# Performance work log

Measured on AMD Instinct MI355X. Metric: run time of the kernel, lower is better.

The kernel has to match this reference:

```python
import jax, jax.numpy as jnp
import numpy as np

C, H, W = 64, 32, 32  # feature planes are (1, 64, 32, 32)
M = 1_048_576         # number of query points


def bilinear_sample(plane, coords):
    """torch.nn.functional.grid_sample, mode='bilinear', padding_mode='zeros',
    align_corners=True, for a single plane.
    plane: (C, H, W); coords: (M, 2) with (x, y) in [-1, 1] convention.
    Returns (M, C)."""
    c, h, w = plane.shape
    # align_corners=True mapping: -1 -> 0, +1 -> size-1
    x = (coords[:, 0] + 1.0) * 0.5 * (w - 1)
    y = (coords[:, 1] + 1.0) * 0.5 * (h - 1)
    x0 = jnp.floor(x)
    y0 = jnp.floor(y)
    wx1 = x - x0
    wy1 = y - y0
    wx0 = 1.0 - wx1
    wy0 = 1.0 - wy1

    def gather(xi, yi):
        xi = xi.astype(jnp.int32)
        yi = yi.astype(jnp.int32)
        valid = (xi >= 0) & (xi < w) & (yi >= 0) & (yi < h)  # zeros padding
        xc = jnp.clip(xi, 0, w - 1)
        yc = jnp.clip(yi, 0, h - 1)
        v = plane[:, yc, xc]  # (C, M)
        return jnp.where(valid[None, :], v, 0.0)

    out = (gather(x0, y0) * (wx0 * wy0)[None, :]
           + gather(x0 + 1, y0) * (wx1 * wy0)[None, :]
           + gather(x0, y0 + 1) * (wx0 * wy1)[None, :]
           + gather(x0 + 1, y0 + 1) * (wx1 * wy1)[None, :])
    return out.T  # (M, C)


def setup_inputs() -> dict:
    key = jax.random.key(0)
    ks = jax.random.split(key, 10)
    coordinates = jax.random.normal(ks[0], (1, M, 3), dtype=jnp.float32)
    # tri-plane embeddings: randn * 0.1, shape (1, C, H, W)
    plane_xy = jax.random.normal(ks[1], (1, C, H, W), dtype=jnp.float32) * 0.1
    plane_yz = jax.random.normal(ks[2], (1, C, H, W), dtype=jnp.float32) * 0.1
    plane_xz = jax.random.normal(ks[3], (1, C, H, W), dtype=jnp.float32) * 0.1
    # MLP 64 -> 128 -> 128 -> 1 (torch Linear weight shape = (out, in))
    # layer 0: first_layer_sine_init -> U(-1/64, 1/64)
    w1 = jax.random.uniform(ks[4], (128, 64), jnp.float32, -1.0 / 64, 1.0 / 64)
    b1 = jnp.zeros((128,), jnp.float32)
    # layers 1,2: frequency_init(30) -> U(-sqrt(6/in)/30, sqrt(6/in)/30)
    s2 = np.sqrt(6.0 / 128) / 30.0
    w2 = jax.random.uniform(ks[5], (128, 128), jnp.float32, -s2, s2)
    b2 = jnp.zeros((128,), jnp.float32)
    w3 = jax.random.uniform(ks[6], (1, 128), jnp.float32, -s2, s2)
    b3 = jnp.zeros((1,), jnp.float32)
    return {"coordinates": coordinates, "plane_xy": plane_xy, "plane_yz": plane_yz,
            "plane_xz": plane_xz, "w1": w1, "b1": b1, "w2": w2, "b2": b2,
            "w3": w3, "b3": b3}


def reference(coordinates, plane_xy, plane_yz, plane_xz, w1, b1, w2, b2, w3, b3):
    # coordinates: (1, M, 3); planes have leading batch dim of 1 (torch requires
    # grid batch == plane batch, so batch_size is structurally 1).
    samp = jax.vmap(bilinear_sample, in_axes=(None, 0))
    xy = samp(plane_xy[0], coordinates[..., 0:2])   # (1, M, C)
    yz = samp(plane_yz[0], coordinates[..., 1:3])   # (1, M, C)
    xz = samp(plane_xz[0], coordinates[..., ::2])   # (1, M, C)
    features = xy * yz * xz                          # aggregate_fn='prod'
    h = jax.nn.relu(jnp.einsum('bmc,oc->bmo', features, w1) + b1)
    h = jax.nn.relu(jnp.einsum('bmc,oc->bmo', h, w2) + b2)
    out = jnp.einsum('bmc,oc->bmo', h, w3) + b3      # (1, M, 1)
    return out
```

## Files before the change

### kernel.cpp

```cpp
#include <hip/hip_runtime.h>

#define MPTS 1048576

typedef _Float16 f16;
typedef _Float16 f16x2 __attribute__((ext_vector_type(2)));
typedef _Float16 f16x4 __attribute__((ext_vector_type(4)));
typedef _Float16 f16x8 __attribute__((ext_vector_type(8)));
typedef float f32x4 __attribute__((ext_vector_type(4)));

static const size_t OFF_Z    = 0;
static const size_t OFF_CNT  = 64;
static const size_t OFF_PL   = 256;
static const size_t OFF_PLD  = OFF_PL + 786432;
static const size_t OFF_W1H  = OFF_PLD + 786432;
static const size_t OFF_W2H  = OFF_W1H + 16384;
static const size_t OFF_BCNT = OFF_W2H + 32768;
static const size_t OFF_BOFF = OFF_BCNT + 4096;
static const size_t OFF_LIST = OFF_BOFF + 4096;
static const size_t OFF_PC   = OFF_LIST + (size_t)MPTS*4;
static const size_t WS_LIST  = OFF_PC;
static const size_t WS_PC    = OFF_PC + (size_t)MPTS*16;

__device__ __forceinline__ int iclamp(int v, int lo, int hi) {
    return v < lo ? lo : (v > hi ? hi : v);
}
__device__ __forceinline__ int imin(int a, int b) { return a < b ? a : b; }

__device__ __forceinline__ bool isact(float x, float y, float z) {
    float px = fmaf(x, 15.5f, 15.5f);
    float py = fmaf(y, 15.5f, 15.5f);
    float pz = fmaf(z, 15.5f, 15.5f);
    return (px > -1.0f) & (px < 32.0f) & (py > -1.0f) & (py < 32.0f) &
           (pz > -1.0f) & (pz < 32.0f);
}

struct Bi { int o00, o01, o10, o11; float w00, w01, w10, w11; };

__device__ __forceinline__ Bi mkbi(float pa, float pb) {
    float fa = floorf(pa), fb = floorf(pb);
    int ia0 = (int)fa, ib0 = (int)fb;
    int ia1 = ia0 + 1, ib1 = ib0 + 1;
    float wa1 = pa - fa, wa0 = 1.0f - wa1;
    float wb1 = pb - fb, wb0 = 1.0f - wb1;
    float va0 = (ia0 >= 0 && ia0 < 32) ? wa0 : 0.0f;
    float va1 = (ia1 >= 0 && ia1 < 32) ? wa1 : 0.0f;
    float vb0 = (ib0 >= 0 && ib0 < 32) ? wb0 : 0.0f;
    float vb1 = (ib1 >= 0 && ib1 < 32) ? wb1 : 0.0f;
    int ca0 = iclamp(ia0, 0, 31), ca1 = iclamp(ia1, 0, 31);
    int cb0 = iclamp(ib0, 0, 31), cb1 = iclamp(ib1, 0, 31);
    Bi r;
    r.o00 = (cb0 * 32 + ca0) * 64; r.o01 = (cb0 * 32 + ca1) * 64;
    r.o10 = (cb1 * 32 + ca0) * 64; r.o11 = (cb1 * 32 + ca1) * 64;
    r.w00 = va0 * vb0; r.w01 = va1 * vb0; r.w10 = va0 * vb1; r.w11 = va1 * vb1;
    return r;
}

__device__ __forceinline__ float4 lerp4d(const f16* __restrict__ base, const int4 P) {
    f16x8 r0 = *(const f16x8*)(base + P.x);
    f16x8 r1 = *(const f16x8*)(base + P.y);
    f16x2 w0 = __builtin_bit_cast(f16x2, P.z);
    f16x2 w1 = __builtin_bit_cast(f16x2, P.w);
    const f16x2* a0 = (const f16x2*)&r0;
    const f16x2* a1 = (const f16x2*)&r1;
    float4 r;
    r.x = __builtin_amdgcn_fdot2(a0[0], w0, __builtin_amdgcn_fdot2(a1[0], w1, 0.0f, false), false);
    r.y = __builtin_amdgcn_fdot2(a0[1], w0, __builtin_amdgcn_fdot2(a1[1], w1, 0.0f, false), false);
    r.z = __builtin_amdgcn_fdot2(a0[2], w0, __builtin_amdgcn_fdot2(a1[2], w1, 0.0f, false), false);
    r.w = __builtin_amdgcn_fdot2(a0[3], w0, __builtin_amdgcn_fdot2(a1[3], w1, 0.0f, false), false);
    return r;
}

__device__ __forceinline__ void samp16(const float* __restrict__ pl,
                                       float pa, float pb, int c0,
                                       float* __restrict__ f, const bool mult) {
    Bi B = mkbi(pa, pb);
    const float4* p00 = (const float4*)(pl + B.o00 + c0);
    const float4* p01 = (const float4*)(pl + B.o01 + c0);
    const float4* p10 = (const float4*)(pl + B.o10 + c0);
    const float4* p11 = (const float4*)(pl + B.o11 + c0);
#pragma unroll
    for (int q = 0; q < 4; ++q) {
        float4 g00 = p00[q], g01 = p01[q], g10 = p10[q], g11 = p11[q];
        float vx = fmaf(B.w00, g00.x, fmaf(B.w01, g01.x, fmaf(B.w10, g10.x, B.w11 * g11.x)));
        float vy = fmaf(B.w00, g00.y, fmaf(B.w01, g01.y, fmaf(B.w10, g10.y, B.w11 * g11.y)));
        float vz = fmaf(B.w00, g00.z, fmaf(B.w01, g01.z, fmaf(B.w10, g10.z, B.w11 * g11.z)));
        float vw = fmaf(B.w00, g00.w, fmaf(B.w01, g01.w, fmaf(B.w10, g10.w, B.w11 * g11.w)));
        if (mult) {
            f[4*q+0] *= vx; f[4*q+1] *= vy; f[4*q+2] *= vz; f[4*q+3] *= vw;
        } else {
            f[4*q+0] = vx; f[4*q+1] = vy; f[4*q+2] = vz; f[4*q+3] = vw;
        }
    }
}

__global__ void k_prep(const float* __restrict__ pxy, const float* __restrict__ pyz,
                       const float* __restrict__ pxz,
                       const float* __restrict__ w1, const float* __restrict__ w2,
                       const float* __restrict__ b1, const float* __restrict__ b2,
                       const float* __restrict__ w3, const float* __restrict__ b3,
                       float* __restrict__ planes, f16* __restrict__ dupl,
                       f16* __restrict__ w1h, f16* __restrict__ w2h,
                       float* __restrict__ zout) {
    if (blockIdx.x == 864) {
        int p = threadIdx.x;
        if (p >= 128) return;
        float h2p = b2[p];
        for (int o = 0; o < 128; ++o) h2p += w2[p * 128 + o] * fmaxf(b1[o], 0.0f);
        __shared__ float red[128];
        red[p] = fmaxf(h2p, 0.0f) * w3[p];
        __syncthreads();
        for (int s = 64; s > 0; s >>= 1) {
            if (p < s) red[p] += red[p + s];
            __syncthreads();
        }
        if (p == 0) *zout = red[0] + b3[0];
        return;
    }
    int tid = blockIdx.x * 256 + threadIdx.x;
    if (tid < 3 * 65536) {
        int t = tid >> 16;
        int r = tid & 65535;
        int hw = r >> 6;
        int c = r & 63;
        int y = hw >> 5, x = hw & 31;
        int xp1 = imin(x + 1, 31);
        const float* src = (t == 0) ? pxy : ((t == 1) ? pyz : pxz);
        float v  = src[c * 1024 + hw];
        float v1 = src[c * 1024 + y * 32 + xp1];
        planes[tid] = v;
        f16* d = dupl + (size_t)t * 131072 + hw * 128 + c * 2;
        d[0] = (f16)v;
        d[1] = (f16)v1;
    } else if (tid < 3 * 65536 + 8192) {
        int r = tid - 3 * 65536;
        w1h[r] = (f16)w1[r];
    } else {
        int r = tid - (3 * 65536 + 8192);
        w2h[r] = (f16)w2[r];
    }
}

__global__ void k_count(const float* __restrict__ coords, const float* __restrict__ zptr,
                        int* __restrict__ bcnt, float* __restrict__ out) {
    int t = threadIdx.x, bid = blockIdx.x;
    const float4* c4 = (const float4*)coords + 768 * (size_t)bid + 3 * t;
    float4 a = c4[0], b = c4[1], c = c4[2];
    int base = bid * 1024 + t * 4;
    float z = *zptr;
    bool a0 = isact(a.x, a.y, a.z);
    bool a1 = isact(a.w, b.x, b.y);
    bool a2 = isact(b.z, b.w, c.x);
    bool a3 = isact(c.y, c.z, c.w);
    if (!a0) out[base + 0] = z;
    if (!a1) out[base + 1] = z;
    if (!a2) out[base + 2] = z;
    if (!a3) out[base + 3] = z;
    int s = (int)a0 + (int)a1 + (int)a2 + (int)a3;
#pragma unroll
    for (int off = 1; off <= 32; off <<= 1) s += __shfl_xor(s, off, 64);
    __shared__ int wt[4];
    if ((t & 63) == 0) wt[t >> 6] = s;
    __syncthreads();
    if (t == 0) bcnt[bid] = wt[0] + wt[1] + wt[2] + wt[3];
}

__global__ void k_scan(const int* __restrict__ bcnt, int* __restrict__ boff,
                       int* __restrict__ cnt) {
    int t = threadIdx.x, lane = t & 63, wv = t >> 6;
    int mine = bcnt[t];
    int incl = mine;
#pragma unroll
    for (int off = 1; off <= 32; off <<= 1) {
        int v = __shfl_up(incl, off, 64);
        if (lane >= off) incl += v;
    }
    __shared__ int wtot[16];
    if (lane == 63) wtot[wv] = incl;
    __syncthreads();
    int wexcl = 0;
#pragma unroll
    for (int k = 0; k < 16; ++k) wexcl += (k < wv) ? wtot[k] : 0;
    boff[t] = wexcl + incl - mine;
    if (t == 1023) *cnt = wexcl + incl;
}

template<bool PC>
__global__ void k_scatter(const float* __restrict__ coords, const int* __restrict__ boff,
                          int* __restrict__ list, float4* __restrict__ pc4) {
    int t = threadIdx.x, bid = blockIdx.x, lane = t & 63, wv = t >> 6;
    const float4* c4 = (const float4*)coords + 768 * (size_t)bid + 3 * t;
    float4 a = c4[0], b = c4[1], c = c4[2];
    int base = bid * 1024 + t * 4;
    float xs[4] = {a.x, a.w, b.z, c.y};
    float ys[4] = {a.y, b.x, b.w, c.z};
    float zs[4] = {a.z, b.y, c.x, c.w};
    bool act[4];
#pragma unroll
    for (int j = 0; j < 4; ++j) act[j] = isact(xs[j], ys[j], zs[j]);
    int mine = (int)act[0] + (int)act[1] + (int)act[2] + (int)act[3];
    int incl = mine;
#pragma unroll
    for (int off = 1; off <= 32; off <<= 1) {
        int v = __shfl_up(incl, off, 64);
        if (lane >= off) incl += v;
    }
    __shared__ int wtot[4];
    if (lane == 63) wtot[wv] = incl;
    __syncthreads();
    int wexcl = 0;
#pragma unroll
    for (int k = 0; k < 4; ++k) wexcl += (k < wv) ? wtot[k] : 0;
    int pos = boff[bid] + wexcl + incl - mine;
#pragma unroll
    for (int j = 0; j < 4; ++j) {
        if (act[j]) {
            list[pos] = base + j;
            if (PC) {
                float4 p;
                p.x = fmaf(xs[j], 15.5f, 15.5f);
                p.y = fmaf(ys[j], 15.5f, 15.5f);
                p.z = fmaf(zs[j], 15.5f, 15.5f);
                p.w = 0.0f;
                pc4[pos] = p;
            }
            ++pos;
        }
    }
}

__global__ __launch_bounds__(256, 2)
void k_fused(const float4* __restrict__ pc4, const f16* __restrict__ dupl,
             const f16* __restrict__ w1h, const f16* __restrict__ w2h,
             const float* __restrict__ b1, const float* __restrict__ b2,
             const float* __restrict__ w3, const float* __restrict__ b3,
             const int* __restrict__ cnt, const int* __restrict__ list,
             float* __restrict__ out) {
    const int n = *cnt;
    const int tile = blockIdx.x;
    if (tile * 64 >= n) return;

    __shared__ __attribute__((aligned(16))) char smem[16384 + 3072];
    f16*   Fs   = (f16*)smem;
    f16*   H1s  = (f16*)smem;
    int4*  BsP  = (int4*)(smem + 16384);
    float* outp = (float*)(smem + 16384);

    const int t   = threadIdx.x;
    const int wv  = t >> 6;
    const int l   = t & 63;
    const int l15 = l & 15;
    const int lg  = l >> 4;
    const int ptw = t >> 4;
    const int cq  = t & 15;

    const float b3v = b3[0];

    if ((t & 3) < 3) {
        int pt0 = t >> 2;
        int pl  = t & 3;
        int ic = imin(tile * 64 + pt0, n - 1);
        float4 c = pc4[ic];
        float pa = (pl == 1) ? c.y : c.x;
        float pb = (pl == 0) ? c.y : c.z;
        float fa = floorf(pa), fb = floorf(pb);
        int ia0 = (int)fa, ib0 = (int)fb;
        float wa1 = pa - fa, wa0 = 1.0f - wa1;
        float wb1 = pb - fb, wb0 = 1.0f - wb1;
        float va0 = (ia0 >= 0 && ia0 < 32) ? wa0 : 0.0f;
        float va1 = (ia0 + 1 >= 0 && ia0 + 1 < 32) ? wa1 : 0.0f;
        float vb0 = (ib0 >= 0 && ib0 < 32) ? wb0 : 0.0f;
        float vb1 = (ib0 + 1 >= 0 && ib0 + 1 < 32) ? wb1 : 0.0f;
        int xb = iclamp(ia0, 0, 31);
        float wx0 = (ia0 < 0) ? va1 : va0;
        float wx1 = (ia0 < 0) ? 0.0f : va1;
        int yb0 = iclamp(ib0, 0, 31), yb1 = iclamp(ib0 + 1, 0, 31);
        f16x2 p0; p0[0] = (f16)(wx0 * vb0); p0[1] = (f16)(wx1 * vb0);
        f16x2 p1; p1[0] = (f16)(wx0 * vb1); p1[1] = (f16)(wx1 * vb1);
        int o0 = (yb0 * 32 + xb) * 128;
        int o1 = (yb1 * 32 + xb) * 128;
        BsP[pt0 * 3 + pl] = make_int4(o0, o1,
                                      __builtin_bit_cast(int, p0),
                                      __builtin_bit_cast(int, p1));
    }
    __syncthreads();

    const f16* bch = dupl + cq * 8;
#pragma unroll
    for (int pass = 0; pass < 4; ++pass) {
        int pt = pass * 16 + ptw;
        float4 s0 = lerp4d(bch,          BsP[pt * 3 + 0]);
        float4 s1 = lerp4d(bch + 131072, BsP[pt * 3 + 1]);
        float4 s2 = lerp4d(bch + 262144, BsP[pt * 3 + 2]);
        float4 f;
        f.x = (s0.x * s1.x) * s2.x;
        f.y = (s0.y * s1.y) * s2.y;
        f.z = (s0.z * s1.z) * s2.z;
        f.w = (s0.w * s1.w) * s2.w;
        f16x4 pk;
        pk[0] = (f16)f.x; pk[1] = (f16)f.y; pk[2] = (f16)f.z; pk[3] = (f16)f.w;
        *(f16x4*)((char*)Fs + pt * 128 + ((cq * 8) ^ ((pt & 7) << 4))) = pk;
    }
    __syncthreads();

    f16x8 af[4][2];
#pragma unroll
    for (int Mt = 0; Mt < 4; ++Mt) {
        int row = Mt * 16 + l15;
        const char* rb = (const char*)Fs + row * 128;
        int sw = (row & 7) << 4;
        af[Mt][0] = *(const f16x8*)(rb + ((lg * 16) ^ sw));
        af[Mt][1] = *(const f16x8*)(rb + ((64 + lg * 16) ^ sw));
    }

    f16x8 wf1[2][2];
    f16x8 wf2[2][4];
    f32x4 b1q[2], b2q[2], w3q[2];
#pragma unroll
    for (int ntl = 0; ntl < 2; ++ntl) {
        int nrow = (wv * 2 + ntl) * 16 + l15;
        wf1[ntl][0] = *(const f16x8*)(w1h + nrow * 64 + lg * 8);
        wf1[ntl][1] = *(const f16x8*)(w1h + nrow * 64 + 32 + lg * 8);
#pragma unroll
        for (int ks = 0; ks < 4; ++ks)
            wf2[ntl][ks] = *(const f16x8*)(w2h + nrow * 128 + ks * 32 + lg * 8);
        int nb = (wv * 2 + ntl) * 16 + lg * 4;
        b1q[ntl] = *(const f32x4*)(b1 + nb);
        b2q[ntl] = *(const f32x4*)(b2 + nb);
        w3q[ntl] = *(const f32x4*)(w3 + nb);
    }
    __syncthreads();

    f32x4 acc[2][4];
#pragma unroll
    for (int ntl = 0; ntl < 2; ++ntl)
#pragma unroll
        for (int Mt = 0; Mt < 4; ++Mt) acc[ntl][Mt] = b1q[ntl];
    __builtin_amdgcn_s_setprio(1);
#pragma unroll
    for (int Mt = 0; Mt < 4; ++Mt) {
#pragma unroll
        for (int ntl = 0; ntl < 2; ++ntl) {
            acc[ntl][Mt] = __builtin_amdgcn_mfma_f32_16x16x32_f16(wf1[ntl][0], af[Mt][0], acc[ntl][Mt], 0, 0, 0);
            acc[ntl][Mt] = __builtin_amdgcn_mfma_f32_16x16x32_f16(wf1[ntl][1], af[Mt][1], acc[ntl][Mt], 0, 0, 0);
        }
    }
    __builtin_amdgcn_s_setprio(0);

#pragma unroll
    for (int ntl = 0; ntl < 2; ++ntl) {
#pragma unroll
        for (int Mt = 0; Mt < 4; ++Mt) {
            int pt = Mt * 16 + l15;
            int off = (((wv * 2 + ntl) * 32 + lg * 8) ^ ((pt & 7) << 4));
            f16x4 h;
            h[0] = (f16)fmaxf(acc[ntl][Mt][0], 0.0f);
            h[1] = (f16)fmaxf(acc[ntl][Mt][1], 0.0f);
            h[2] = (f16)fmaxf(acc[ntl][Mt][2], 0.0f);
            h[3] = (f16)fmaxf(acc[ntl][Mt][3], 0.0f);
            *(f16x4*)((char*)H1s + pt * 256 + off) = h;
        }
    }
    __syncthreads();

    f32x4 acc2[2][4];
#pragma unroll
    for (int ntl = 0; ntl < 2; ++ntl)
#pragma unroll
        for (int Mt = 0; Mt < 4; ++Mt) acc2[ntl][Mt] = b2q[ntl];
#pragma unroll
    for (int Mt = 0; Mt < 4; ++Mt) {
        int row = Mt * 16 + l15;
        const char* rb = (const char*)H1s + row * 256;
        int sw = (row & 7) << 4;
        f16x8 a0 = *(const f16x8*)(rb + ((lg * 16) ^ sw));
        f16x8 a1 = *(const f16x8*)(rb + ((64 + lg * 16) ^ sw));
        f16x8 a2 = *(const f16x8*)(rb + ((128 + lg * 16) ^ sw));
        f16x8 a3 = *(const f16x8*)(rb + ((192 + lg * 16) ^ sw));
        __builtin_amdgcn_s_setprio(1);
#pragma unroll
        for (int ntl = 0; ntl < 2; ++ntl) {
            acc2[ntl][Mt] = __builtin_amdgcn_mfma_f32_16x16x32_f16(wf2[ntl][0], a0, acc2[ntl][Mt], 0, 0, 0);
            acc2[ntl][Mt] = __builtin_amdgcn_mfma_f32_16x16x32_f16(wf2[ntl][1], a1, acc2[ntl][Mt], 0, 0, 0);
            acc2[ntl][Mt] = __builtin_amdgcn_mfma_f32_16x16x32_f16(wf2[ntl][2], a2, acc2[ntl][Mt], 0, 0, 0);
            acc2[ntl][Mt] = __builtin_amdgcn_mfma_f32_16x16x32_f16(wf2[ntl][3], a3, acc2[ntl][Mt], 0, 0, 0);
        }
        __builtin_amdgcn_s_setprio(0);
    }

#pragma unroll
    for (int Mt = 0; Mt < 4; ++Mt) {
        float s = 0.0f;
#pragma unroll
        for (int ntl = 0; ntl < 2; ++ntl)
#pragma unroll
            for (int r = 0; r < 4; ++r)
                s = fmaf(fmaxf(acc2[ntl][Mt][r], 0.0f), w3q[ntl][r], s);
        s += __shfl_xor(s, 16, 64);
        s += __shfl_xor(s, 32, 64);
        if (lg == 0) outp[wv * 64 + Mt * 16 + l15] = s;
    }
    __syncthreads();
    if (t < 64) {
        int gi = tile * 64 + t;
        if (gi < n) {
            float s = outp[0 * 64 + t] + outp[1 * 64 + t] +
                      outp[2 * 64 + t] + outp[3 * 64 + t] + b3v;
            out[list[gi]] = s;
        }
    }
}

__global__ __launch_bounds__(256, 2)
void k_mlp(const float* __restrict__ coords, const float* __restrict__ planes,
           const f16* __restrict__ w1h, const f16* __restrict__ w2h,
           const float* __restrict__ b1, const float* __restrict__ b2,
           const float* __restrict__ w3, const float* __restrict__ b3,
           const int* __restrict__ cnt, const int* __restrict__ list,
           float* __restrict__ out) {
    const int n = *cnt;
    const int tile = blockIdx.x;
    if (tile * 64 >= n) return;

    __shared__ __attribute__((aligned(16))) f16 Fs[64 * 64];
    __shared__ __attribute__((aligned(16))) f16 H1s[64 * 128];
    __shared__ float outp[4][64];

    const int t   = threadIdx.x;
    const int wv  = t >> 6;
    const int l   = t & 63;
    const int l15 = l & 15;
    const int lg  = l >> 4;

    const float* pl0 = planes;
    const float* pl1 = planes + 65536;
    const float* pl2 = planes + 131072;

    f16x8 wf1[2][2];
    f16x8 wf2[2][4];
    float b1v[2], b2v[2], w3v[2];
#pragma unroll
    for (int ntl = 0; ntl < 2; ++ntl) {
        int nrow = (wv * 2 + ntl) * 16 + l15;
#pragma unroll
        for (int ks = 0; ks < 2; ++ks)
            wf1[ntl][ks] = *(const f16x8*)(w1h + nrow * 64 + ks * 32 + lg * 8);
#pragma unroll
        for (int ks = 0; ks < 4; ++ks)
            wf2[ntl][ks] = *(const f16x8*)(w2h + nrow * 128 + ks * 32 + lg * 8);
        b1v[ntl] = b1[nrow];
        b2v[ntl] = b2[nrow];
        w3v[ntl] = w3[nrow];
    }
    const float b3v = b3[0];

    {
        int pt = t >> 2, c0 = (t & 3) * 16;
        int ic = imin(tile * 64 + pt, n - 1);
        int i = list[ic];
        float px = fmaf(coords[3 * i + 0], 15.5f, 15.5f);
        float py = fmaf(coords[3 * i + 1], 15.5f, 15.5f);
        float pz = fmaf(coords[3 * i + 2], 15.5f, 15.5f);
        float feat[16];
        samp16(pl0, px, py, c0, feat, false);
        samp16(pl1, py, pz, c0, feat, true);
        samp16(pl2, px, pz, c0, feat, true);
        int sw = (pt & 7) << 4;
        char* Fb = (char*)Fs + pt * 128;
        f16x8 pk;
#pragma unroll
        for (int j = 0; j < 8; ++j) pk[j] = (f16)feat[j];
        *(f16x8*)(Fb + ((c0 * 2) ^ sw)) = pk;
#pragma unroll
        for (int j = 0; j < 8; ++j) pk[j] = (f16)feat[8 + j];
        *(f16x8*)(Fb + ((c0 * 2 + 16) ^ sw)) = pk;
    }
    __syncthreads();

    f32x4 acc[2][4];
#pragma unroll
    for (int ntl = 0; ntl < 2; ++ntl) {
        f32x4 ini = {b1v[ntl], b1v[ntl], b1v[ntl], b1v[ntl]};
#pragma unroll
        for (int Mt = 0; Mt < 4; ++Mt) acc[ntl][Mt] = ini;
    }
#pragma unroll
    for (int Mt = 0; Mt < 4; ++Mt) {
        int row = Mt * 16 + l15;
        const char* rb = (const char*)Fs + row * 128;
        int sw = (row & 7) << 4;
        f16x8 a0 = *(const f16x8*)(rb + ((lg * 16) ^ sw));
        f16x8 a1 = *(const f16x8*)(rb + ((64 + lg * 16) ^ sw));
#pragma unroll
        for (int ntl = 0; ntl < 2; ++ntl) {
            acc[ntl][Mt] = __builtin_amdgcn_mfma_f32_16x16x32_f16(a0, wf1[ntl][0], acc[ntl][Mt], 0, 0, 0);
            acc[ntl][Mt] = __builtin_amdgcn_mfma_f32_16x16x32_f16(a1, wf1[ntl][1], acc[ntl][Mt], 0, 0, 0);
        }
    }
#pragma unroll
    for (int ntl = 0; ntl < 2; ++ntl) {
        int ncol = (wv * 2 + ntl) * 16 + l15;
#pragma unroll
        for (int Mt = 0; Mt < 4; ++Mt) {
#pragma unroll
            for (int r = 0; r < 4; ++r) {
                int prow = Mt * 16 + lg * 4 + r;
                float v = fmaxf(acc[ntl][Mt][r], 0.0f);
                *(f16*)((char*)H1s + prow * 256 + ((ncol * 2) ^ ((prow & 7) << 4))) = (f16)v;
            }
        }
    }
    __syncthreads();

    f32x4 acc2[2][4];
#pragma unroll
    for (int ntl = 0; ntl < 2; ++ntl) {
        f32x4 ini = {b2v[ntl], b2v[ntl], b2v[ntl], b2v[ntl]};
#pragma unroll
        for (int Mt = 0; Mt < 4; ++Mt) acc2[ntl][Mt] = ini;
    }
#pragma unroll
    for (int Mt = 0; Mt < 4; ++Mt) {
        int row = Mt * 16 + l15;
        const char* rb = (const char*)H1s + row * 256;
        int sw = (row & 7) << 4;
        f16x8 a0 = *(const f16x8*)(rb + ((lg * 16) ^ sw));
        f16x8 a1 = *(const f16x8*)(rb + ((64 + lg * 16) ^ sw));
        f16x8 a2 = *(const f16x8*)(rb + ((128 + lg * 16) ^ sw));
        f16x8 a3 = *(const f16x8*)(rb + ((192 + lg * 16) ^ sw));
#pragma unroll
        for (int ntl = 0; ntl < 2; ++ntl) {
            acc2[ntl][Mt] = __builtin_amdgcn_mfma_f32_16x16x32_f16(a0, wf2[ntl][0], acc2[ntl][Mt], 0, 0, 0);
            acc2[ntl][Mt] = __builtin_amdgcn_mfma_f32_16x16x32_f16(a1, wf2[ntl][1], acc2[ntl][Mt], 0, 0, 0);
            acc2[ntl][Mt] = __builtin_amdgcn_mfma_f32_16x16x32_f16(a2, wf2[ntl][2], acc2[ntl][Mt], 0, 0, 0);
            acc2[ntl][Mt] = __builtin_amdgcn_mfma_f32_16x16x32_f16(a3, wf2[ntl][3], acc2[ntl][Mt], 0, 0, 0);
        }
    }

    float part[4][4];
#pragma unroll
    for (int Mt = 0; Mt < 4; ++Mt)
#pragma unroll
        for (int r = 0; r < 4; ++r)
            part[Mt][r] = fmaxf(acc2[0][Mt][r], 0.0f) * w3v[0] +
                          fmaxf(acc2[1][Mt][r], 0.0f) * w3v[1];
#pragma unroll
    for (int off = 1; off <= 8; off <<= 1) {
#pragma unroll
        for (int Mt = 0; Mt < 4; ++Mt)
#pragma unroll
            for (int r = 0; r < 4; ++r)
                part[Mt][r] += __shfl_xor(part[Mt][r], off, 64);
    }
    if (l15 == 0) {
#pragma unroll
        for (int Mt = 0; Mt < 4; ++Mt)
#pragma unroll
            for (int r = 0; r < 4; ++r)
                outp[wv][Mt * 16 + lg * 4 + r] = part[Mt][r];
    }
    __syncthreads();
    if (t < 64) {
        int gi = tile * 64 + t;
        if (gi < n) {
            float s = outp[0][t] + outp[1][t] + outp[2][t] + outp[3][t] + b3v;
            out[list[gi]] = s;
        }
    }
}

__global__ void k_fallback(const float* __restrict__ coords,
                           const float* __restrict__ p0, const float* __restrict__ p1,
                           const float* __restrict__ p2,
                           const float* __restrict__ w1, const float* __restrict__ b1,
                           const float* __restrict__ w2, const float* __restrict__ b2,
                           const float* __restrict__ w3, const float* __restrict__ b3,
                           float* __restrict__ out) {
    int i = blockIdx.x * 256 + threadIdx.x;
    if (i >= MPTS) return;
    float x = coords[3 * i + 0], y = coords[3 * i + 1], z = coords[3 * i + 2];
    float px = fmaf(x, 15.5f, 15.5f);
    float py = fmaf(y, 15.5f, 15.5f);
    float pz = fmaf(z, 15.5f, 15.5f);
    float feat[64];
    const float* pls[3] = {p0, p1, p2};
    float pa[3] = {px, py, px}, pb[3] = {py, pz, pz};
    for (int pidx = 0; pidx < 3; ++pidx) {
        float paf = pa[pidx], pbf = pb[pidx];
        float fa = floorf(paf), fb = floorf(pbf);
        int ia0 = (int)fa, ib0 = (int)fb, ia1 = ia0 + 1, ib1 = ib0 + 1;
        float wa1 = paf - fa, wa0 = 1.0f - wa1, wb1 = pbf - fb, wb0 = 1.0f - wb1;
        float va0 = (ia0 >= 0 && ia0 < 32) ? wa0 : 0.0f;
        float va1 = (ia1 >= 0 && ia1 < 32) ? wa1 : 0.0f;
        float vb0 = (ib0 >= 0 && ib0 < 32) ? wb0 : 0.0f;
        float vb1 = (ib1 >= 0 && ib1 < 32) ? wb1 : 0.0f;
        int ca0 = iclamp(ia0, 0, 31), ca1 = iclamp(ia1, 0, 31);
        int cb0 = iclamp(ib0, 0, 31), cb1 = iclamp(ib1, 0, 31);
        float w00 = va0 * vb0, w01 = va1 * vb0, w10 = va0 * vb1, w11 = va1 * vb1;
        int o00 = cb0 * 32 + ca0, o01 = cb0 * 32 + ca1;
        int o10 = cb1 * 32 + ca0, o11 = cb1 * 32 + ca1;
        const float* pl = pls[pidx];
        for (int c = 0; c < 64; ++c) {
            const float* pc = pl + c * 1024;
            float v = fmaf(w00, pc[o00], fmaf(w01, pc[o01],
                      fmaf(w10, pc[o10], w11 * pc[o11])));
            if (pidx == 0) feat[c] = v; else feat[c] *= v;
        }
    }
    float oa = b3[0];
    for (int half = 0; half < 2; ++half) {
        float h2h[64];
        for (int p = 0; p < 64; ++p) h2h[p] = b2[half * 64 + p];
        for (int o = 0; o < 128; ++o) {
            float a = b1[o];
            for (int c = 0; c < 64; ++c) a = fmaf(feat[c], w1[o * 64 + c], a);
            float r = fmaxf(a, 0.0f);
            for (int p = 0; p < 64; ++p) h2h[p] = fmaf(r, w2[(half * 64 + p) * 128 + o], h2h[p]);
        }
        for (int p = 0; p < 64; ++p) oa = fmaf(fmaxf(h2h[p], 0.0f), w3[half * 64 + p], oa);
    }
    out[i] = oa;
}

extern "C" void kernel_launch(void* const* d_in, const int* in_sizes, int n_in,
                              void* d_out, int out_size, void* d_ws, size_t ws_size,
                              hipStream_t stream) {
    const float* coords = (const float*)d_in[0];
    const float* pxy    = (const float*)d_in[1];
    const float* pyz    = (const float*)d_in[2];
    const float* pxz    = (const float*)d_in[3];
    const float* w1     = (const float*)d_in[4];
    const float* b1     = (const float*)d_in[5];
    const float* w2     = (const float*)d_in[6];
    const float* b2     = (const float*)d_in[7];
    const float* w3     = (const float*)d_in[8];
    const float* b3     = (const float*)d_in[9];
    float* out = (float*)d_out;

    if (ws_size >= WS_LIST) {
        float*  zout   = (float*)((char*)d_ws + OFF_Z);
        int*    cnt    = (int*)((char*)d_ws + OFF_CNT);
        float*  planes = (float*)((char*)d_ws + OFF_PL);
        f16*    dupl   = (f16*)((char*)d_ws + OFF_PLD);
        f16*    w1h    = (f16*)((char*)d_ws + OFF_W1H);
        f16*    w2h    = (f16*)((char*)d_ws + OFF_W2H);
        int*    bcnt   = (int*)((char*)d_ws + OFF_BCNT);
        int*    boff   = (int*)((char*)d_ws + OFF_BOFF);
        int*    list   = (int*)((char*)d_ws + OFF_LIST);
        float4* pc4    = (float4*)((char*)d_ws + OFF_PC);

        k_prep<<<865, 256, 0, stream>>>(pxy, pyz, pxz, w1, w2, b1, b2, w3, b3,
                                        planes, dupl, w1h, w2h, zout);
        k_count<<<1024, 256, 0, stream>>>(coords, zout, bcnt, out);
        k_scan<<<1, 1024, 0, stream>>>(bcnt, boff, cnt);

        if (ws_size >= WS_PC) {
            k_scatter<true><<<1024, 256, 0, stream>>>(coords, boff, list, pc4);
            k_fused<<<16384, 256, 0, stream>>>(pc4, dupl, w1h, w2h,
                                               b1, b2, w3, b3, cnt, list, out);
        } else {
            k_scatter<false><<<1024, 256, 0, stream>>>(coords, boff, list, nullptr);
            k_mlp<<<16384, 256, 0, stream>>>(coords, planes, w1h, w2h,
                                             b1, b2, w3, b3, cnt, list, out);
        }
    } else {
        k_fallback<<<4096, 256, 0, stream>>>(coords, pxy, pyz, pxz,
                                             w1, b1, w2, b2, w3, b3, out);
    }
}
```

Baseline: 84.50 us.

## Fuse count, scan and scatter into one decoupled-lookback classify kernel

Replaces the three-kernel count/scan/scatter compaction with a single pass. Each block publishes its active count to a flag array, then spins on the flags of all earlier blocks to get its output offset. This removes two launches and a second read of the coordinates, at the cost of a memset and a spin-wait that relies on earlier blocks being scheduled first (forward progress is not guaranteed). It also skips writing the fp32 plane copy when the precomputed-coordinate path is used.

```diff
diff --git a/kernel.cpp b/kernel.cpp
--- a/kernel.cpp
+++ b/kernel.cpp
@@ -14,9 +14,8 @@
 static const size_t OFF_PLD  = OFF_PL + 786432;
 static const size_t OFF_W1H  = OFF_PLD + 786432;
 static const size_t OFF_W2H  = OFF_W1H + 16384;
-static const size_t OFF_BCNT = OFF_W2H + 32768;
-static const size_t OFF_BOFF = OFF_BCNT + 4096;
-static const size_t OFF_LIST = OFF_BOFF + 4096;
+static const size_t OFF_BFLG = OFF_W2H + 32768;
+static const size_t OFF_LIST = OFF_BFLG + 4096;
 static const size_t OFF_PC   = OFF_LIST + (size_t)MPTS*4;
 static const size_t WS_LIST  = OFF_PC;
 static const size_t WS_PC    = OFF_PC + (size_t)MPTS*16;
@@ -100,7 +99,7 @@
                        const float* __restrict__ w3, const float* __restrict__ b3,
                        float* __restrict__ planes, f16* __restrict__ dupl,
                        f16* __restrict__ w1h, f16* __restrict__ w2h,
-                       float* __restrict__ zout) {
+                       float* __restrict__ zout, int wplanes) {
     if (blockIdx.x == 864) {
         int p = threadIdx.x;
         if (p >= 128) return;
@@ -127,7 +126,7 @@
         const float* src = (t == 0) ? pxy : ((t == 1) ? pyz : pxz);
         float v  = src[c * 1024 + hw];
         float v1 = src[c * 1024 + y * 32 + xp1];
-        planes[tid] = v;
+        if (wplanes) planes[tid] = v;
         f16* d = dupl + (size_t)t * 131072 + hw * 128 + c * 2;
         d[0] = (f16)v;
         d[1] = (f16)v1;
@@ -140,53 +139,12 @@
     }
 }
 
-__global__ void k_count(const float* __restrict__ coords, const float* __restrict__ zptr,
-                        int* __restrict__ bcnt, float* __restrict__ out) {
-    int t = threadIdx.x, bid = blockIdx.x;
-    const float4* c4 = (const float4*)coords + 768 * (size_t)bid + 3 * t;
-    float4 a = c4[0], b = c4[1], c = c4[2];
-    int base = bid * 1024 + t * 4;
-    float z = *zptr;
-    bool a0 = isact(a.x, a.y, a.z);
-    bool a1 = isact(a.w, b.x, b.y);
-    bool a2 = isact(b.z, b.w, c.x);
-    bool a3 = isact(c.y, c.z, c.w);
-    if (!a0) out[base + 0] = z;
-    if (!a1) out[base + 1] = z;
-    if (!a2) out[base + 2] = z;
-    if (!a3) out[base + 3] = z;
-    int s = (int)a0 + (int)a1 + (int)a2 + (int)a3;
-#pragma unroll
-    for (int off = 1; off <= 32; off <<= 1) s += __shfl_xor(s, off, 64);
-    __shared__ int wt[4];
-    if ((t & 63) == 0) wt[t >> 6] = s;
-    __syncthreads();
-    if (t == 0) bcnt[bid] = wt[0] + wt[1] + wt[2] + wt[3];
-}
-
-__global__ void k_scan(const int* __restrict__ bcnt, int* __restrict__ boff,
-                       int* __restrict__ cnt) {
-    int t = threadIdx.x, lane = t & 63, wv = t >> 6;
-    int mine = bcnt[t];
-    int incl = mine;
-#pragma unroll
-    for (int off = 1; off <= 32; off <<= 1) {
-        int v = __shfl_up(incl, off, 64);
-        if (lane >= off) incl += v;
-    }
-    __shared__ int wtot[16];
-    if (lane == 63) wtot[wv] = incl;
-    __syncthreads();
-    int wexcl = 0;
-#pragma unroll
-    for (int k = 0; k < 16; ++k) wexcl += (k < wv) ? wtot[k] : 0;
-    boff[t] = wexcl + incl - mine;
-    if (t == 1023) *cnt = wexcl + incl;
-}
-
 template<bool PC>
-__global__ void k_scatter(const float* __restrict__ coords, const int* __restrict__ boff,
-                          int* __restrict__ list, float4* __restrict__ pc4) {
+__global__ void k_classify(const float* __restrict__ coords,
+                           const float* __restrict__ zptr,
+                           int* __restrict__ bflag, int* __restrict__ cnt,
+                           int* __restrict__ list, float4* __restrict__ pc4,
+                           float* __restrict__ out) {
     int t = threadIdx.x, bid = blockIdx.x, lane = t & 63, wv = t >> 6;
     const float4* c4 = (const float4*)coords + 768 * (size_t)bid + 3 * t;
     float4 a = c4[0], b = c4[1], c = c4[2];
@@ -198,6 +156,7 @@
 #pragma unroll
     for (int j = 0; j < 4; ++j) act[j] = isact(xs[j], ys[j], zs[j]);
     int mine = (int)act[0] + (int)act[1] + (int)act[2] + (int)act[3];
+
     int incl = mine;
 #pragma unroll
     for (int off = 1; off <= 32; off <<= 1) {
@@ -205,12 +164,36 @@
         if (lane >= off) incl += v;
     }
     __shared__ int wtot[4];
+    __shared__ int pw[4];
     if (lane == 63) wtot[wv] = incl;
     __syncthreads();
+    int btot = wtot[0] + wtot[1] + wtot[2] + wtot[3];
+
+    if (t == 0) atomicExch(&bflag[bid], btot + 1);
+
+    int pre = 0;
+    for (int i = t; i < bid; i += 256) {
+        int v;
+        do { v = atomicAdd(&bflag[i], 0); } while (v == 0);
+        pre += v - 1;
+    }
+#pragma unroll
+    for (int off = 1; off <= 32; off <<= 1) pre += __shfl_xor(pre, off, 64);
+    if (lane == 0) pw[wv] = pre;
+    __syncthreads();
+    int boffv = pw[0] + pw[1] + pw[2] + pw[3];
+
+    if (bid == 1023 && t == 0) *cnt = boffv + btot;
+
+    float z = *zptr;
+#pragma unroll
+    for (int j = 0; j < 4; ++j)
+        if (!act[j]) out[base + j] = z;
+
     int wexcl = 0;
 #pragma unroll
     for (int k = 0; k < 4; ++k) wexcl += (k < wv) ? wtot[k] : 0;
-    int pos = boff[bid] + wexcl + incl - mine;
+    int pos = boffv + wexcl + incl - mine;
 #pragma unroll
     for (int j = 0; j < 4; ++j) {
         if (act[j]) {
@@ -643,22 +626,22 @@
         f16*    dupl   = (f16*)((char*)d_ws + OFF_PLD);
         f16*    w1h    = (f16*)((char*)d_ws + OFF_W1H);
         f16*    w2h    = (f16*)((char*)d_ws + OFF_W2H);
-        int*    bcnt   = (int*)((char*)d_ws + OFF_BCNT);
-        int*    boff   = (int*)((char*)d_ws + OFF_BOFF);
+        int*    bflag  = (int*)((char*)d_ws + OFF_BFLG);
         int*    list   = (int*)((char*)d_ws + OFF_LIST);
         float4* pc4    = (float4*)((char*)d_ws + OFF_PC);
-
+        const bool pc  = (ws_size >= WS_PC);
+
+        hipMemsetAsync(bflag, 0, 4096, stream);
         k_prep<<<865, 256, 0, stream>>>(pxy, pyz, pxz, w1, w2, b1, b2, w3, b3,
-                                        planes, dupl, w1h, w2h, zout);
-        k_count<<<1024, 256, 0, stream>>>(coords, zout, bcnt, out);
-        k_scan<<<1, 1024, 0, stream>>>(bcnt, boff, cnt);
-
-        if (ws_size >= WS_PC) {
-            k_scatter<true><<<1024, 256, 0, stream>>>(coords, boff, list, pc4);
+                                        planes, dupl, w1h, w2h, zout, pc ? 0 : 1);
+        if (pc) {
+            k_classify<true><<<1024, 256, 0, stream>>>(coords, zout, bflag, cnt,
+                                                       list, pc4, out);
             k_fused<<<16384, 256, 0, stream>>>(pc4, dupl, w1h, w2h,
                                                b1, b2, w3, b3, cnt, list, out);
         } else {
-            k_scatter<false><<<1024, 256, 0, stream>>>(coords, boff, list, nullptr);
+            k_classify<false><<<1024, 256, 0, stream>>>(coords, zout, bflag, cnt,
+                                                        list, nullptr, out);
             k_mlp<<<16384, 256, 0, stream>>>(coords, planes, w1h, w2h,
                                              b1, b2, w3, b3, cnt, list, out);
         }
```

Result: slower. 88.41 us (+4.6%).
